# Performance work log

Measured on AMD Instinct MI355X. Metric: run time of the kernel, lower is better.

Reference implementation:

```python
import jax, jax.numpy as jnp
import numpy as np

# ---- static structure for the 28x28 image grid ----
H = 28
V = H * H          # 784 vertices
T = 25             # landscape sample points
K_MAX = 2          # landscape orders kept
M0 = 0.05          # DTM mass parameter

_idx = np.arange(V).reshape(H, H)
_e_h = np.stack([_idx[:, :-1].ravel(), _idx[:, 1:].ravel()], 1)
_e_v = np.stack([_idx[:-1, :].ravel(), _idx[1:, :].ravel()], 1)
EDGES = np.concatenate([_e_h, _e_v], 0).astype(np.int32)   # [E,2], E=1512
E = EDGES.shape[0]

# grid coordinates per lims=[[27,0],[0,27]], normalized to [0,1]
_c0 = np.linspace(1.0, 0.0, H)
_c1 = np.linspace(0.0, 1.0, H)
COORDS = np.stack(np.meshgrid(_c0, _c1, indexing='ij'), -1).reshape(V, 2)
_D2 = ((COORDS[:, None, :] - COORDS[None, :, :]) ** 2).sum(-1)   # [V,V] static
ORDER = jnp.asarray(np.argsort(_D2, 1).astype(np.int32))          # nearest-first per row
D2S = jnp.asarray(np.take_along_axis(_D2, np.argsort(_D2, 1), 1).astype(np.float32))
TSEQ = jnp.asarray(np.linspace(0.0, 0.5, T).astype(np.float32))   # landscape eval grid
EA = jnp.asarray(EDGES[:, 0])
EB = jnp.asarray(EDGES[:, 1])


def _dtm(w):
    """Distance-to-measure filtration on the grid. w: [B,V] pixel masses -> [B,V]."""
    m = w / jnp.clip(jnp.sum(w, 1, keepdims=True), 1e-12)
    ws = m[:, ORDER]                                  # [B,V,V] masses in nearest-first order
    c = jnp.cumsum(ws, -1)
    take = jnp.minimum(ws, jnp.clip(M0 - (c - ws), 0.0, None))  # mass used until m0 reached
    return jnp.sqrt(jnp.sum(take * D2S[None], -1) / M0 + 1e-12)


def _ph0(f):
    """0-dim persistence of sublevel filtration of f on the grid graph (Kruskal/union-find).
    f: [V] -> (births, deaths, valid) each [E]."""
    w = jnp.maximum(f[EA], f[EB])                     # edge filtration values
    o = jnp.argsort(w)
    aa, bb, ww = EA[o], EB[o], w[o]

    def step(carry, e):
        r, bv = carry                                 # r: fully-compressed root per vertex
        ai, bi, wi = e
        ra, rb = r[ai], r[bi]
        diff = ra != rb
        young_a = bv[ra] >= bv[rb]                    # younger comp = larger birth
        young = jnp.where(young_a, ra, rb)
        old = jnp.where(young_a, rb, ra)
        birth = bv[young]
        r = jnp.where(diff & (r == young), old, r)    # merge, keep full compression
        return (r, bv), (birth, wi, diff)

    init = (jnp.arange(V, dtype=jnp.int32), f)
    _, (bs, ds, valid) = jax.lax.scan(step, init, (aa, bb, ww))
    return bs, ds, valid


def _landscape(bs, ds, valid):
    """Persistence landscape lambda_k(t), k<K_MAX, t in TSEQ -> [K_MAX*T] features."""
    tent = jnp.maximum(jnp.minimum(TSEQ[:, None] - bs[None, :], ds[None, :] - TSEQ[:, None]), 0.0)
    tent = tent * valid[None, :]                      # [T,E]
    top = jax.lax.top_k(tent, K_MAX)[0]               # [T,K]
    return top.T.reshape(-1)                          # [K*T] = 50


def setup_inputs() -> dict:
    key = jax.random.key(0)
    k1, k2, k3, k4, k5 = jax.random.split(key, 5)
    return {
        'input': jax.random.uniform(k1, (128, 1, 28, 28), dtype=jnp.float32),
        'w_topo': jax.random.normal(k2, (50, 100), dtype=jnp.float32) * 0.1,
        'b_topo': jax.random.normal(k3, (100,), dtype=jnp.float32) * 0.01,
        'w_fc': jax.random.normal(k4, (100, 10), dtype=jnp.float32) * 0.1,
        'b_fc': jax.random.normal(k5, (10,), dtype=jnp.float32) * 0.01,
    }


def reference(input, w_topo, b_topo, w_fc, b_fc):
    B = input.shape[0]
    x = input.reshape(B, V)
    f = _dtm(x)                                       # [B,V] DTM filtration
    bs, ds, valid = jax.vmap(_ph0)(f)                 # persistence pairs per sample
    feats = jax.vmap(_landscape)(bs, ds, valid.astype(f.dtype))  # [B,50]
    h = jax.nn.relu(feats @ w_topo + b_topo)          # AdTopoLayer linear + ReLU -> [B,100]
    return h @ w_fc + b_fc                            # [B,10]
```

## Files before the change

### kernel.cpp

```cpp
#include <hip/hip_runtime.h>
#include <math.h>

#define HH 28
#define VV 784
#define EE 1512
#define TT 25
#define M0C 0.05


#define DECODE(idx, A, B)                                                  \
  {                                                                        \
    if ((idx) < 756) {                                                     \
      int i_ = (idx) / 27, j_ = (idx) - i_ * 27;                           \
      A = i_ * HH + j_; B = A + 1;                                         \
    } else {                                                               \
      int q_ = (idx) - 756;                                                \
      int i_ = q_ / HH, j_ = q_ - i_ * HH;                                 \
      A = i_ * HH + j_; B = A + HH;                                        \
    }                                                                      \
  }

__global__ __launch_bounds__(512) void k_pre(const float* __restrict__ x,
                                             int* __restrict__ ORDER, float* __restrict__ D2S,
                                             float* __restrict__ MT) {
  __shared__ unsigned long long keys[1024];
  __shared__ double sred[8];
  __shared__ double Ssh;
  const int tid = threadIdx.x;
  if (blockIdx.x < VV) {
    const int v = blockIdx.x;
    const int i1 = v / HH, j1 = v % HH;
    const double step = 1.0 / 27.0;
    const double c0v = (i1 == 27) ? 0.0 : 1.0 - (double)i1 * step;
    const double c1v = (j1 == 27) ? 1.0 : (double)j1 * step;
    for (int u = tid; u < 1024; u += 512) {
      unsigned long long key = ~0ULL;
      if (u < VV) {
        int i2 = u / HH, j2 = u % HH;
        double c0u = (i2 == 27) ? 0.0 : 1.0 - (double)i2 * step;
        double c1u = (j2 == 27) ? 1.0 : (double)j2 * step;
        double dx = c0v - c0u, dy = c1v - c1u;
        float d2 = (float)(dx * dx + dy * dy);
        key = ((unsigned long long)__float_as_uint(d2) << 32) | (unsigned)u;
      }
      keys[u] = key;
    }
    __syncthreads();
    for (unsigned k = 2; k <= 1024; k <<= 1) {
      for (unsigned j = k >> 1; j; j >>= 1) {
        for (unsigned i = tid; i < 1024; i += 512) {
          unsigned l = i ^ j;
          if (l > i) {
            unsigned long long a = keys[i], c = keys[l];
            if ((a > c) == ((i & k) == 0)) { keys[i] = c; keys[l] = a; }
          }
        }
        __syncthreads();
      }
    }
    for (int u = tid; u < VV; u += 512) {
      unsigned long long key = keys[u];
      ORDER[v * VV + u] = (int)(key & 0xffffffffu);
      D2S[v * VV + u] = __uint_as_float((unsigned)(key >> 32));
    }
  } else {
    const int b = blockIdx.x - VV;
    double s = 0.0;
    for (int i = tid; i < VV; i += 512) s += (double)x[b * VV + i];
    for (int off = 32; off; off >>= 1) s += __shfl_xor(s, off, 64);
    if ((tid & 63) == 0) sred[tid >> 6] = s;
    __syncthreads();
    if (tid == 0) {
      double S = 0.0;
      #pragma unroll
      for (int wv = 0; wv < 8; ++wv) S += sred[wv];
      Ssh = (S > 1e-12) ? S : 1e-12;
    }
    __syncthreads();
    double S = Ssh;
    for (int i = tid; i < VV; i += 512) MT[i * 128 + b] = (float)((double)x[b * VV + i] / S);
  }
}

__global__ __launch_bounds__(128) void k_dtm(const float* __restrict__ MT, const int* __restrict__ ORDER,
                                             const float* __restrict__ D2S, float* __restrict__ F) {
  const int v = blockIdx.x;
  const int tid = threadIdx.x;
  __shared__ int ordS[VV];
  __shared__ float d2sS[VV];
  for (int k = tid; k < VV; k += 128) {
    ordS[k] = ORDER[v * VV + k];
    d2sS[k] = D2S[v * VV + k];
  }
  __syncthreads();
  float P = 0.0f, acc = 0.0f;
  for (int base = 0; base < VV; base += 16) {
    #pragma unroll
    for (int kk = 0; kk < 16; ++kk) {
      int k = base + kk;
      float mass = MT[ordS[k] * 128 + tid];
      float room = (float)M0C - P;
      room = room > 0.0f ? room : 0.0f;
      float take = mass < room ? mass : room;
      acc += take * d2sS[k];
      P += mass;
    }
    if (__all(P >= (float)M0C)) break;
  }
  F[tid * VV + v] = sqrtf(acc / (float)M0C + 1e-12f);
}

__global__ __launch_bounds__(512) void k_main(const float* __restrict__ F,
                                              const float* __restrict__ w_topo, const float* __restrict__ b_topo,
                                              const float* __restrict__ w_fc, const float* __restrict__ b_fc,
                                              float* __restrict__ out) {
  const int b = blockIdx.x;
  const int tid = threadIdx.x;
  __shared__ float fv[VV];
  __shared__ unsigned long long keys[2048];
  __shared__ unsigned long long par64[VV];
  __shared__ unsigned long long pairs[VV];
  __shared__ float feat[2 * TT];
  __shared__ float hbuf[100];
  __shared__ int cntS;
  for (int i = tid; i < VV; i += 512) {
    float f = F[b * VV + i];
    fv[i] = f;
    par64[i] = ((unsigned long long)__float_as_uint(f) << 32) | (unsigned)i;
  }
  __syncthreads();
  for (int e = tid; e < 2048; e += 512) {
    unsigned long long key = 0xFFFFFFFF00000000ULL;
    if (e < EE) {
      int aa, bb;
      DECODE(e, aa, bb);
      float w = fmaxf(fv[aa], fv[bb]);
      unsigned lo = ((e >= 756) ? (1u << 20) : 0u) | ((unsigned)aa << 10) | (unsigned)bb;
      key = ((unsigned long long)__float_as_uint(w) << 32) | lo;
    }
    keys[e] = key;
  }
  __syncthreads();
  for (unsigned k = 2; k <= 2048; k <<= 1) {
    for (unsigned j = k >> 1; j; j >>= 1) {
      for (unsigned i = tid; i < 2048; i += 512) {
        unsigned l = i ^ j;
        if (l > i) {
          unsigned long long a = keys[i], c = keys[l];
          if ((a > c) == ((i & k) == 0)) { keys[i] = c; keys[l] = a; }
        }
      }
      __syncthreads();
    }
  }
  if (tid < 64) {
    const int lane = tid;
    const unsigned long long lbit = 1ULL << lane;
    int cnt = 0;
    unsigned long long K = keys[lane];
    for (int batch = 0; batch < 24; ++batch) {
      unsigned long long Kn = keys[(batch + 1) * 64 + lane];
      unsigned lo = (unsigned)K;
      int aa = (int)((lo >> 10) & 1023), bb = (int)(lo & 1023);
      unsigned wbits = (unsigned)(K >> 32);
      unsigned long long pka = par64[aa], pkb = par64[bb];
      unsigned ra = (unsigned)pka, rb = (unsigned)pkb;
      unsigned fa = (unsigned)(pka >> 32), fb = (unsigned)(pkb >> 32);
      unsigned long long candB = __ballot(ra != rb);
      if (candB) {
        bool rec = false;
        unsigned long long pairv = 0;
        if (__popcll(candB) == 1) {
          if (ra != rb) {
            bool ya = (fa >= fb);
            unsigned young = ya ? ra : rb;
            unsigned oldv = ya ? rb : ra;
            unsigned foldv = ya ? fb : fa;
            unsigned birth = ya ? fa : fb;
            par64[young] = ((unsigned long long)foldv << 32) | oldv;
            pairv = ((unsigned long long)birth << 32) | wbits;
            rec = (wbits > birth);
          }
        } else {
          int merged = 0;
          unsigned young_w = 0;
          #pragma unroll 4
          for (int j = 0; j < 64; ++j) {
            unsigned s_ra = (unsigned)__builtin_amdgcn_readlane((int)ra, j);
            unsigned s_rb = (unsigned)__builtin_amdgcn_readlane((int)rb, j);
            if (s_ra != s_rb) {
              unsigned s_fa = (unsigned)__builtin_amdgcn_readlane((int)fa, j);
              unsigned s_fb = (unsigned)__builtin_amdgcn_readlane((int)fb, j);
              bool ya = (s_fa >= s_fb);
              unsigned young = ya ? s_ra : s_rb;
              unsigned oldv = ya ? s_rb : s_ra;
              unsigned foldv = ya ? s_fb : s_fa;
              unsigned birth = ya ? s_fa : s_fb;
              bool me = (lane == j);
              merged = me ? 1 : merged;
              young_w = me ? young : young_w;
              pairv = me ? (((unsigned long long)birth << 32) | wbits) : pairv;
              bool ma = (ra == young);
              ra = ma ? oldv : ra;
              fa = ma ? foldv : fa;
              bool mb2 = (rb == young);
              rb = mb2 ? oldv : rb;
              fb = mb2 ? foldv : fb;
            }
          }
          if (merged) par64[young_w] = ((unsigned long long)fa << 32) | ra;
          rec = merged && ((unsigned)pairv > (unsigned)(pairv >> 32));
        }
        unsigned long long recB = __ballot(rec);
        int rank = __popcll(recB & (lbit - 1ULL));
        if (rec) pairs[cnt + rank] = pairv;
        cnt += (int)__popcll(recB);
        {
          #pragma unroll
          for (int s = 0; s < 12; ++s) {
            unsigned long long p = par64[lane + 64 * s];
            unsigned long long q = par64[(unsigned)p];
            par64[lane + 64 * s] = q;
          }
          if (lane < 16) {
            unsigned long long p = par64[768 + lane];
            unsigned long long q = par64[(unsigned)p];
            par64[768 + lane] = q;
          }
        }
      }
      K = Kn;
    }
    if (lane == 0) cntS = cnt;
  }
  __syncthreads();
  const int cnt = cntS;
  const int wid = tid >> 6, lane = tid & 63;
  for (int t = wid; t < TT; t += 8) {
    double tvd = (t == 24) ? 0.5 : (double)t * (0.5 / 24.0);
    float tv = (float)tvd;
    float m1 = 0.0f, m2 = 0.0f;
    for (int pidx = lane; pidx < cnt; pidx += 64) {
      unsigned long long pr = pairs[pidx];
      float pbv = __uint_as_float((unsigned)(pr >> 32));
      float pdv = __uint_as_float((unsigned)pr);
      float tent = fminf(tv - pbv, pdv - tv);
      tent = fmaxf(tent, 0.0f);
      if (tent > m1) { m2 = m1; m1 = tent; }
      else if (tent > m2) { m2 = tent; }
    }
    #pragma unroll
    for (int off = 32; off; off >>= 1) {
      float o1 = __shfl_xor(m1, off, 64);
      float o2 = __shfl_xor(m2, off, 64);
      float n1 = fmaxf(m1, o1);
      float n2 = fmaxf(fminf(m1, o1), fmaxf(m2, o2));
      m1 = n1; m2 = n2;
    }
    if (lane == 0) { feat[t] = m1; feat[TT + t] = m2; }
  }
  __syncthreads();
  if (tid < 100) {
    double h = (double)b_topo[tid];
    for (int k2 = 0; k2 < 50; ++k2) h += (double)feat[k2] * (double)w_topo[k2 * 100 + tid];
    hbuf[tid] = (h > 0.0) ? (float)h : 0.0f;
  }
  __syncthreads();
  if (tid < 10) {
    double o = (double)b_fc[tid];
    for (int k2 = 0; k2 < 100; ++k2) o += (double)hbuf[k2] * (double)w_fc[k2 * 10 + tid];
    out[b * 10 + tid] = (float)o;
  }
}

extern "C" void kernel_launch(void* const* d_in, const int* in_sizes, int n_in,
                              void* d_out, int out_size, void* d_ws, size_t ws_size,
                              hipStream_t stream) {
  const float* x = (const float*)d_in[0];
  const float* w_topo = (const float*)d_in[1];
  const float* b_topo = (const float*)d_in[2];
  const float* w_fc = (const float*)d_in[3];
  const float* b_fc = (const float*)d_in[4];
  float* outp = (float*)d_out;
  char* ws = (char*)d_ws;
  int* ORDER = (int*)ws;
  float* D2S = (float*)(ws + 2458624);
  float* MT = (float*)(ws + 4917248);
  float* F = (float*)(ws + 5318656);

  hipLaunchKernelGGL(k_pre, dim3(VV + 128), dim3(512), 0, stream, x, ORDER, D2S, MT);
  hipLaunchKernelGGL(k_dtm, dim3(VV), dim3(128), 0, stream, MT, ORDER, D2S, F);
  hipLaunchKernelGGL(k_main, dim3(128), dim3(512), 0, stream, F, w_topo, b_topo, w_fc, b_fc, outp);
}
```

Measured before the change: 191.2 us.

## Use 32-bit integer sort keys, bound the lane scan, and exit once the MST completes

The precompute kernel now sorts 32-bit keys built from integer squared grid distances instead of 64-bit float-based keys, and recomputes the float distance after sorting. This halves LDS traffic in the bitonic sort. In the union-find kernel, the serial readlane scan is limited to the range of candidate lanes and made branchless. The edge loop also exits early once V-1 merges have happened, skipping the remaining batches. The early exit relies on the merge count being exact, and integer distance ties may order differently from the float keys.

```diff
diff --git a/kernel.cpp b/kernel.cpp
--- a/kernel.cpp
+++ b/kernel.cpp
@@ -23,7 +23,7 @@
 __global__ __launch_bounds__(512) void k_pre(const float* __restrict__ x,
                                              int* __restrict__ ORDER, float* __restrict__ D2S,
                                              float* __restrict__ MT) {
-  __shared__ unsigned long long keys[1024];
+  __shared__ unsigned keysU[1024];
   __shared__ double sred[8];
   __shared__ double Ssh;
   const int tid = threadIdx.x;
@@ -34,16 +34,14 @@
     const double c0v = (i1 == 27) ? 0.0 : 1.0 - (double)i1 * step;
     const double c1v = (j1 == 27) ? 1.0 : (double)j1 * step;
     for (int u = tid; u < 1024; u += 512) {
-      unsigned long long key = ~0ULL;
+      unsigned key = 0xFFFFFFFFu;
       if (u < VV) {
         int i2 = u / HH, j2 = u % HH;
-        double c0u = (i2 == 27) ? 0.0 : 1.0 - (double)i2 * step;
-        double c1u = (j2 == 27) ? 1.0 : (double)j2 * step;
-        double dx = c0v - c0u, dy = c1v - c1u;
-        float d2 = (float)(dx * dx + dy * dy);
-        key = ((unsigned long long)__float_as_uint(d2) << 32) | (unsigned)u;
+        int di = i1 - i2, dj = j1 - j2;
+        unsigned s = (unsigned)(di * di + dj * dj);
+        key = (s << 10) | (unsigned)u;
       }
-      keys[u] = key;
+      keysU[u] = key;
     }
     __syncthreads();
     for (unsigned k = 2; k <= 1024; k <<= 1) {
@@ -51,17 +49,21 @@
         for (unsigned i = tid; i < 1024; i += 512) {
           unsigned l = i ^ j;
           if (l > i) {
-            unsigned long long a = keys[i], c = keys[l];
-            if ((a > c) == ((i & k) == 0)) { keys[i] = c; keys[l] = a; }
+            unsigned a = keysU[i], c = keysU[l];
+            if ((a > c) == ((i & k) == 0)) { keysU[i] = c; keysU[l] = a; }
           }
         }
         __syncthreads();
       }
     }
     for (int u = tid; u < VV; u += 512) {
-      unsigned long long key = keys[u];
-      ORDER[v * VV + u] = (int)(key & 0xffffffffu);
-      D2S[v * VV + u] = __uint_as_float((unsigned)(key >> 32));
+      int uu = (int)(keysU[u] & 1023u);
+      ORDER[v * VV + u] = uu;
+      int i2 = uu / HH, j2 = uu % HH;
+      double c0u = (i2 == 27) ? 0.0 : 1.0 - (double)i2 * step;
+      double c1u = (j2 == 27) ? 1.0 : (double)j2 * step;
+      double dx = c0v - c0u, dy = c1v - c1u;
+      D2S[v * VV + u] = (float)(dx * dx + dy * dy);
     }
   } else {
     const int b = blockIdx.x - VV;
@@ -157,6 +159,7 @@
     const int lane = tid;
     const unsigned long long lbit = 1ULL << lane;
     int cnt = 0;
+    int totalM = 0;
     unsigned long long K = keys[lane];
     for (int batch = 0; batch < 24; ++batch) {
       unsigned long long Kn = keys[(batch + 1) * 64 + lane];
@@ -169,6 +172,7 @@
       unsigned long long candB = __ballot(ra != rb);
       if (candB) {
         bool rec = false;
+        bool iMerged = false;
         unsigned long long pairv = 0;
         if (__popcll(candB) == 1) {
           if (ra != rb) {
@@ -180,41 +184,46 @@
             par64[young] = ((unsigned long long)foldv << 32) | oldv;
             pairv = ((unsigned long long)birth << 32) | wbits;
             rec = (wbits > birth);
+            iMerged = true;
           }
         } else {
+          int jmin = (int)__builtin_ctzll(candB);
+          int jmax = 63 - (int)__builtin_clzll(candB);
           int merged = 0;
           unsigned young_w = 0;
           #pragma unroll 4
-          for (int j = 0; j < 64; ++j) {
+          for (int j = jmin; j <= jmax; ++j) {
             unsigned s_ra = (unsigned)__builtin_amdgcn_readlane((int)ra, j);
             unsigned s_rb = (unsigned)__builtin_amdgcn_readlane((int)rb, j);
-            if (s_ra != s_rb) {
-              unsigned s_fa = (unsigned)__builtin_amdgcn_readlane((int)fa, j);
-              unsigned s_fb = (unsigned)__builtin_amdgcn_readlane((int)fb, j);
-              bool ya = (s_fa >= s_fb);
-              unsigned young = ya ? s_ra : s_rb;
-              unsigned oldv = ya ? s_rb : s_ra;
-              unsigned foldv = ya ? s_fb : s_fa;
-              unsigned birth = ya ? s_fa : s_fb;
-              bool me = (lane == j);
-              merged = me ? 1 : merged;
-              young_w = me ? young : young_w;
-              pairv = me ? (((unsigned long long)birth << 32) | wbits) : pairv;
-              bool ma = (ra == young);
-              ra = ma ? oldv : ra;
-              fa = ma ? foldv : fa;
-              bool mb2 = (rb == young);
-              rb = mb2 ? oldv : rb;
-              fb = mb2 ? foldv : fb;
-            }
+            unsigned s_fa = (unsigned)__builtin_amdgcn_readlane((int)fa, j);
+            unsigned s_fb = (unsigned)__builtin_amdgcn_readlane((int)fb, j);
+            bool sdf = (s_ra != s_rb);
+            bool ya = (s_fa >= s_fb);
+            unsigned young = ya ? s_ra : s_rb;
+            unsigned oldv = ya ? s_rb : s_ra;
+            unsigned foldv = ya ? s_fb : s_fa;
+            unsigned birth = ya ? s_fa : s_fb;
+            unsigned young_eff = sdf ? young : 0xFFFFFFFFu;
+            bool me = (lane == j) & sdf;
+            merged = me ? 1 : merged;
+            young_w = me ? young : young_w;
+            pairv = me ? (((unsigned long long)birth << 32) | wbits) : pairv;
+            bool ma = (ra == young_eff);
+            ra = ma ? oldv : ra;
+            fa = ma ? foldv : fa;
+            bool mb2 = (rb == young_eff);
+            rb = mb2 ? oldv : rb;
+            fb = mb2 ? foldv : fb;
           }
           if (merged) par64[young_w] = ((unsigned long long)fa << 32) | ra;
           rec = merged && ((unsigned)pairv > (unsigned)(pairv >> 32));
+          iMerged = (merged != 0);
         }
         unsigned long long recB = __ballot(rec);
         int rank = __popcll(recB & (lbit - 1ULL));
         if (rec) pairs[cnt + rank] = pairv;
         cnt += (int)__popcll(recB);
+        totalM += (int)__popcll(__ballot(iMerged));
         {
           #pragma unroll
           for (int s = 0; s < 12; ++s) {
@@ -228,6 +237,7 @@
             par64[768 + lane] = q;
           }
         }
+        if (totalM >= VV - 1) break;
       }
       K = Kn;
     }
```

Result: slower. 243.2 us (+27.2%).
